# Kernel tuning notes

Hardware: AMD Instinct MI355X
Metric: run time of the kernel (lower is better)

The kernel has to match this reference:

```python
import jax, jax.numpy as jnp
import numpy as np

B, S, H, E = 8, 512, 1024, 8
T = B * S            # total tokens
CAP = T // E         # capacity, capacity_factor = 1.0


def _moe(x, wg, ew1, eb1, ew2, eb2):
    # x: [T, H] tokens; top-1 gating with capacity, DeepSpeed-style dispatch/combine
    gates = jax.nn.softmax(x @ wg)                      # [T, E]
    idx = jnp.argmax(gates, axis=-1)                    # [T]
    mask1 = jax.nn.one_hot(idx, E, dtype=x.dtype)       # [T, E]
    locations = jnp.cumsum(mask1, axis=0) - 1.0         # position within expert queue
    mask1 = mask1 * (locations < CAP).astype(x.dtype)   # drop overflow tokens
    gates1 = jnp.sum(gates * mask1, axis=-1)            # [T] combine weight
    locs = jnp.sum(locations * mask1, axis=-1).astype(jnp.int32)  # [T]
    loc_oh = jax.nn.one_hot(locs, CAP, dtype=x.dtype)   # [T, C]
    combine = gates1[:, None, None] * mask1[:, :, None] * loc_oh[:, None, :]  # [T,E,C]
    dispatch = (combine > 0).astype(x.dtype)            # [T, E, C]
    xd = jnp.einsum('sec,sm->ecm', dispatch, x)         # gather tokens per expert
    h = jnp.einsum('ecm,emn->ecn', xd, ew1) + eb1[:, None, :]
    h = jnp.einsum('ecn,enp->ecp', h, ew2) + eb2[:, None, :]
    return jnp.einsum('sec,ecm->sm', combine, h)        # scatter back, weighted


def setup_inputs() -> dict:
    key = jax.random.key(0)
    ks = jax.random.split(key, 16)
    w = lambda k, shape: jax.random.normal(k, shape, jnp.float32) * 0.02
    return {
        'x': jax.random.normal(ks[0], (B, S, H), jnp.float32),
        'y': jax.random.randint(ks[1], (B,), 0, H),
        'w1': w(ks[2], (H, H)), 'b1': jnp.zeros((H,), jnp.float32),
        'w2': w(ks[3], (H, H)), 'b2': jnp.zeros((H,), jnp.float32),
        'w3': w(ks[4], (H, H)), 'b3': jnp.zeros((H,), jnp.float32),
        'wg1': w(ks[5], (H, E)),
        'e1_w1': w(ks[6], (E, H, H)), 'e1_b1': jnp.zeros((E, H), jnp.float32),
        'e1_w2': w(ks[7], (E, H, H)), 'e1_b2': jnp.zeros((E, H), jnp.float32),
        'wg2': w(ks[8], (H, E)),
        'e2_w1': w(ks[9], (E, H, H)), 'e2_b1': jnp.zeros((E, H), jnp.float32),
        'e2_w2': w(ks[10], (E, H, H)), 'e2_b2': jnp.zeros((E, H), jnp.float32),
    }


def reference(x, y, w1, b1, w2, b2, w3, b3, wg1, e1_w1, e1_b1, e1_w2, e1_b2,
              wg2, e2_w1, e2_b1, e2_w2, e2_b2):
    xf = x.reshape(-1, H)                               # [T, H]
    hidden = xf @ w1 + b1
    out = _moe(hidden, wg1, e1_w1, e1_b1, e1_w2, e1_b2)
    out = out @ w2 + b2
    out = _moe(out, wg2, e2_w1, e2_b1, e2_w2, e2_b2)
    out = out @ w3 + b3
    hidden = hidden + out
    sent = hidden.reshape(B, S, H).mean(axis=1)         # [B, H] logits
    logp = jax.nn.log_softmax(sent, axis=-1)
    return -jnp.mean(logp[jnp.arange(B), y])
```

## Files before the change

### kernel.cpp

```cpp
#include <hip/hip_runtime.h>

#define TOK 4096
#define HID 1024
#define NEXP 8
#define CAP 512
#define WSZ 1048576

typedef _Float16 f16;
typedef f16 f16x8 __attribute__((ext_vector_type(8)));
typedef f16 f16x4 __attribute__((ext_vector_type(4)));
typedef f16 f16x2 __attribute__((ext_vector_type(2)));
typedef float f32x4 __attribute__((ext_vector_type(4)));

typedef const __attribute__((address_space(1))) void gvoid;
typedef __attribute__((address_space(3))) void lvoid;

__device__ __forceinline__ void gld16(const void* g, void* l) {
  __builtin_amdgcn_global_load_lds((gvoid*)g, (lvoid*)l, 16, 0, 0);
}

template<int MODE>
__global__ __launch_bounds__(512, 1) void gemm_fused(
    const f16* __restrict__ A, const f16* __restrict__ Bt,
    const float* __restrict__ bias, f16* __restrict__ C,
    const int* __restrict__ rowmap, const float* __restrict__ gmax,
    int rowsPerExpert, long bStride, int biasStride,
    const float* __restrict__ tsrc, f16* __restrict__ tdst, int nGemm)
{
  __shared__ __align__(16) unsigned char smem[65536];
  const int tid = threadIdx.x;

  if ((int)blockIdx.x >= nGemm) {
    float (*t)[65] = (float (*)[65])smem;
    const int tb = blockIdx.x - nGemm;
    const int mat = tb >> 7, t7 = tb & 127;
    const int nb = (t7 & 7) * 128, kb = (t7 >> 3) * 64;
    const float* src = tsrc + (size_t)mat * WSZ;
    f16* d = tdst + (size_t)mat * WSZ;
    const int half = tid >> 8, tl = tid & 255;
    const int rr = tl >> 4, c4 = (tl & 15) * 4;
    float (*th)[65] = t + half * 64;
    float4 v[4];
    #pragma unroll
    for (int p = 0; p < 4; ++p)
      v[p] = *(const float4*)&src[(size_t)(kb + p * 16 + rr) * HID + nb + half * 64 + c4];
    #pragma unroll
    for (int p = 0; p < 4; ++p) {
      th[p * 16 + rr][c4 + 0] = v[p].x;
      th[p * 16 + rr][c4 + 1] = v[p].y;
      th[p * 16 + rr][c4 + 2] = v[p].z;
      th[p * 16 + rr][c4 + 3] = v[p].w;
    }
    __syncthreads();
    #pragma unroll
    for (int it = 0; it < 2; ++it) {
      const int p = it * 256 + tl;
      const int n = p >> 3, kc = p & 7;
      f16x8 o;
      #pragma unroll
      for (int j = 0; j < 8; ++j) o[j] = (f16)th[kc * 8 + j][n];
      *(f16x8*)&d[(size_t)(nb + half * 64 + n) * HID + kb + kc * 8] = o;
    }
    return;
  }

  f16* As0 = (f16*)smem;
  f16* Bs0 = (f16*)(smem + 32768);
  const int w = tid >> 6, l = tid & 63;
  const int wr = w >> 2, wc = w & 3;

  const int orig = blockIdx.x;
  const int sw = (orig & 7) * 32 + (orig >> 3);
  const int bx = sw & 7, by = sw >> 3;
  const int e = (by * 128) / rowsPerExpert;

  const int lr = l >> 3;
  const int chunkSw = ((l & 7) ^ lr) * 8;

  const f16* pst[4];
  if (w < 4) {
    #pragma unroll
    for (int i = 0; i < 4; ++i) {
      int r = by * 128 + w * 32 + i * 8 + lr;
      long tok = r;
      if (MODE == 1) { int t = rowmap[r]; tok = (t < 0) ? (long)TOK : (long)t; }
      pst[i] = A + tok * HID + chunkSw;
    }
  } else {
    #pragma unroll
    for (int i = 0; i < 4; ++i)
      pst[i] = Bt + (size_t)e * bStride
             + (size_t)(bx * 128 + (w - 4) * 32 + i * 8 + lr) * HID + chunkSw;
  }

  f32x4 acc[4][2];
  #pragma unroll
  for (int i = 0; i < 4; ++i)
    #pragma unroll
    for (int j = 0; j < 2; ++j) acc[i][j] = (f32x4){0.f, 0.f, 0.f, 0.f};

  const int g = l >> 4, c = l & 15, sa = c & 7;

  {
    f16* db = (w < 4) ? As0 + (w * 32) * 64 : Bs0 + ((w - 4) * 32) * 64;
    #pragma unroll
    for (int i = 0; i < 4; ++i) gld16(pst[i], db + i * 8 * 64);
  }

  int cur = 0;
  for (int t = 0; t < 15; ++t) {
    {
      const int k0 = (t + 1) * 64;
      f16* db = (w < 4) ? As0 + ((cur ^ 1) * 8192) + (w * 32) * 64
                        : Bs0 + ((cur ^ 1) * 8192) + ((w - 4) * 32) * 64;
      #pragma unroll
      for (int i = 0; i < 4; ++i) gld16(pst[i] + k0, db + i * 8 * 64);
    }
    asm volatile("s_waitcnt vmcnt(4)" ::: "memory");
    asm volatile("s_barrier" ::: "memory");
    __builtin_amdgcn_s_setprio(1);
    #pragma unroll
    for (int h = 0; h < 2; ++h) {
      const int q = ((h * 4 + g) ^ sa) * 8;
      f16x8 af[4], bf[2];
      #pragma unroll
      for (int mi = 0; mi < 4; ++mi)
        af[mi] = *(const f16x8*)&As0[cur * 8192 + (wr * 64 + mi * 16 + c) * 64 + q];
      #pragma unroll
      for (int ni = 0; ni < 2; ++ni)
        bf[ni] = *(const f16x8*)&Bs0[cur * 8192 + (wc * 32 + ni * 16 + c) * 64 + q];
      #pragma unroll
      for (int mi = 0; mi < 4; ++mi)
        #pragma unroll
        for (int ni = 0; ni < 2; ++ni)
          acc[mi][ni] = __builtin_amdgcn_mfma_f32_16x16x32_f16(
              af[mi], bf[ni], acc[mi][ni], 0, 0, 0);
    }
    __builtin_amdgcn_s_setprio(0);
    asm volatile("s_barrier" ::: "memory");
    cur ^= 1;
  }
  asm volatile("s_waitcnt vmcnt(0)" ::: "memory");
  asm volatile("s_barrier" ::: "memory");
  __builtin_amdgcn_s_setprio(1);
  #pragma unroll
  for (int h = 0; h < 2; ++h) {
    const int q = ((h * 4 + g) ^ sa) * 8;
    f16x8 af[4], bf[2];
    #pragma unroll
    for (int mi = 0; mi < 4; ++mi)
      af[mi] = *(const f16x8*)&As0[cur * 8192 + (wr * 64 + mi * 16 + c) * 64 + q];
    #pragma unroll
    for (int ni = 0; ni < 2; ++ni)
      bf[ni] = *(const f16x8*)&Bs0[cur * 8192 + (wc * 32 + ni * 16 + c) * 64 + q];
    #pragma unroll
    for (int mi = 0; mi < 4; ++mi)
      #pragma unroll
      for (int ni = 0; ni < 2; ++ni)
        acc[mi][ni] = __builtin_amdgcn_mfma_f32_16x16x32_f16(
            af[mi], bf[ni], acc[mi][ni], 0, 0, 0);
  }
  __builtin_amdgcn_s_setprio(0);

  int tk[4][4];
  float gv[4][4];
  if (MODE == 2) {
    #pragma unroll
    for (int mi = 0; mi < 4; ++mi)
      #pragma unroll
      for (int rr = 0; rr < 4; ++rr) {
        int r = by * 128 + wr * 64 + mi * 16 + g * 4 + rr;
        int t = rowmap[r];
        tk[mi][rr] = t;
        gv[mi][rr] = (t >= 0) ? gmax[t] : 0.f;
      }
  }
  #pragma unroll
  for (int ni = 0; ni < 2; ++ni) {
    const int col = bx * 128 + wc * 32 + ni * 16 + c;
    const float bv = bias[(size_t)e * biasStride + col];
    #pragma unroll
    for (int mi = 0; mi < 4; ++mi) {
      #pragma unroll
      for (int rr = 0; rr < 4; ++rr) {
        const float v = acc[mi][ni][rr] + bv;
        if (MODE == 2) {
          if (tk[mi][rr] >= 0)
            C[(size_t)tk[mi][rr] * HID + col] = (f16)(v * gv[mi][rr]);
        } else {
          const int row = by * 128 + wr * 64 + mi * 16 + g * 4 + rr;
          C[(size_t)row * HID + col] = (f16)v;
        }
      }
    }
  }
}

__global__ __launch_bounds__(256, 8) void tcast3(
    const float* __restrict__ w1, const float* __restrict__ w2,
    const float* __restrict__ w3, f16* __restrict__ dst)
{
  __shared__ float t[64][65];
  const int z = blockIdx.z;
  const float* src = (z == 0) ? w1 : (z == 1) ? w2 : w3;
  f16* d = dst + (size_t)z * WSZ;
  const int tid = threadIdx.x;
  const int kb = blockIdx.y * 64, nb = blockIdx.x * 64;
  const int rr = tid >> 4, c4 = (tid & 15) * 4;
  float4 v[4];
  #pragma unroll
  for (int p = 0; p < 4; ++p)
    v[p] = *(const float4*)&src[(size_t)(kb + p * 16 + rr) * HID + nb + c4];
  #pragma unroll
  for (int p = 0; p < 4; ++p) {
    t[p * 16 + rr][c4 + 0] = v[p].x;
    t[p * 16 + rr][c4 + 1] = v[p].y;
    t[p * 16 + rr][c4 + 2] = v[p].z;
    t[p * 16 + rr][c4 + 3] = v[p].w;
  }
  __syncthreads();
  #pragma unroll
  for (int half = 0; half < 2; ++half) {
    const int p = half * 256 + tid;
    const int n = p >> 3, kc = p & 7;
    f16x8 o;
    #pragma unroll
    for (int j = 0; j < 8; ++j) o[j] = (f16)t[kc * 8 + j][n];
    *(f16x8*)&d[(size_t)(nb + n) * HID + kb + kc * 8] = o;
  }
}

__global__ void prep(const float* __restrict__ x, f16* __restrict__ X0,
                     f16* __restrict__ c1, f16* __restrict__ c2,
                     f16* __restrict__ p1, f16* __restrict__ p2) {
  const size_t i = (size_t)blockIdx.x * 256 + threadIdx.x;
  float4 v = *(const float4*)&x[i * 4];
  f16x4 o = {(f16)v.x, (f16)v.y, (f16)v.z, (f16)v.w};
  *(f16x4*)&X0[i * 4] = o;
  const f16x8 zz = {0, 0, 0, 0, 0, 0, 0, 0};
  if (i < 524288) { ((f16x8*)c1)[i] = zz; ((f16x8*)c2)[i] = zz; }
  if (i < 128)    { ((f16x8*)p1)[i] = zz; ((f16x8*)p2)[i] = zz; }
}

__global__ __launch_bounds__(256) void gate_kernel(
    const f16* __restrict__ act, const float* __restrict__ wg,
    int* __restrict__ idx, float* __restrict__ gmax)
{
  const int tid = threadIdx.x;
  const int tok = blockIdx.x * 8 + (tid >> 5);
  const int sl = tid & 31;
  const f16* row = act + (size_t)tok * HID + sl * 32;
  float xv[32];
  #pragma unroll
  for (int v = 0; v < 4; ++v) {
    f16x8 hv = *(const f16x8*)(row + v * 8);
    #pragma unroll
    for (int j = 0; j < 8; ++j) xv[v * 8 + j] = (float)hv[j];
  }
  float p[NEXP];
  #pragma unroll
  for (int e = 0; e < NEXP; ++e) p[e] = 0.f;
  const float* wr_ = wg + (size_t)(sl * 32) * NEXP;
  #pragma unroll
  for (int j = 0; j < 32; ++j) {
    #pragma unroll
    for (int e = 0; e < NEXP; ++e) p[e] += xv[j] * wr_[j * NEXP + e];
  }
  #pragma unroll
  for (int m = 1; m < 32; m <<= 1) {
    #pragma unroll
    for (int e = 0; e < NEXP; ++e) p[e] += __shfl_xor(p[e], m, 64);
  }
  if (sl == 0) {
    float mx = p[0]; int am = 0;
    #pragma unroll
    for (int e = 1; e < NEXP; ++e)
      if (p[e] > mx) { mx = p[e]; am = e; }
    float s = 0.f;
    #pragma unroll
    for (int e = 0; e < NEXP; ++e) s += expf(p[e] - mx);
    idx[tok] = am;
    gmax[tok] = 1.f / s;
  }
}

__global__ __launch_bounds__(512) void scan_kernel(
    const int* __restrict__ idx, int* __restrict__ rowmap)
{
  __shared__ int sidx[TOK];
  const int tid = threadIdx.x;
  for (int i = tid; i < TOK; i += 512) sidx[i] = idx[i];
  for (int i = tid; i < NEXP * CAP; i += 512) rowmap[i] = -1;
  __syncthreads();
  const int wave = tid >> 6, lane = tid & 63;
  int running = 0;
  for (int ch = 0; ch < TOK / 64; ++ch) {
    int t = ch * 64 + lane;
    bool flag = (sidx[t] == wave);
    unsigned long long m = __ballot(flag);
    int pos = running + __popcll(m & ((1ull << lane) - 1ull));
    if (flag && pos < CAP) rowmap[wave * CAP + pos] = t;
    running += __popcll(m);
  }
}

__global__ __launch_bounds__(256) void mean1_kernel(
    const f16* __restrict__ a, const f16* __restrict__ c,
    float* __restrict__ partial)
{
  const int h2 = blockIdx.x * 256 + threadIdx.x;
  const int b = blockIdx.y, sc = blockIdx.z;
  const f16x2* pa = (const f16x2*)(a + ((size_t)b * 512 + sc * 32) * HID) + h2;
  const f16x2* pc = (const f16x2*)(c + ((size_t)b * 512 + sc * 32) * HID) + h2;
  float a0 = 0.f, a1 = 0.f;
  #pragma unroll 4
  for (int s = 0; s < 32; ++s) {
    f16x2 va = pa[(size_t)s * 512];
    f16x2 vc = pc[(size_t)s * 512];
    a0 += (float)va[0] + (float)vc[0];
    a1 += (float)va[1] + (float)vc[1];
  }
  float* o = partial + ((size_t)sc * 8 + b) * HID;
  o[h2 * 2]     = a0;
  o[h2 * 2 + 1] = a1;
}

__global__ __launch_bounds__(256) void mean2_kernel(
    const float* __restrict__ partial, float* __restrict__ sent)
{
  const int h2 = blockIdx.x * 256 + threadIdx.x;
  const int b = blockIdx.y;
  float a0 = 0.f, a1 = 0.f;
  #pragma unroll
  for (int sc = 0; sc < 16; ++sc) {
    const float* p = partial + ((size_t)sc * 8 + b) * HID + h2 * 2;
    a0 += p[0]; a1 += p[1];
  }
  sent[b * HID + h2 * 2]     = a0 * (1.f / 512.f);
  sent[b * HID + h2 * 2 + 1] = a1 * (1.f / 512.f);
}

__global__ __launch_bounds__(1024) void loss_kernel(
    const float* __restrict__ sent, const int* __restrict__ y,
    float* __restrict__ out)
{
  __shared__ float red[1024];
  float loss = 0.0f;
  for (int b = 0; b < 8; ++b) {
    float v = sent[b * HID + threadIdx.x];
    red[threadIdx.x] = v;
    __syncthreads();
    for (int s = 512; s > 0; s >>= 1) {
      if (threadIdx.x < s)
        red[threadIdx.x] = fmaxf(red[threadIdx.x], red[threadIdx.x + s]);
      __syncthreads();
    }
    float m = red[0];
    __syncthreads();
    red[threadIdx.x] = expf(v - m);
    __syncthreads();
    for (int s = 512; s > 0; s >>= 1) {
      if (threadIdx.x < s) red[threadIdx.x] += red[threadIdx.x + s];
      __syncthreads();
    }
    if (threadIdx.x == 0) {
      float lse = m + logf(red[0]);
      loss += -(sent[b * HID + y[b]] - lse);
    }
    __syncthreads();
  }
  if (threadIdx.x == 0) out[0] = loss * (1.0f / 8.0f);
}

extern "C" void kernel_launch(void* const* d_in, const int* in_sizes, int n_in,
                              void* d_out, int out_size, void* d_ws, size_t ws_size,
                              hipStream_t stream)
{
  const float* x    = (const float*)d_in[0];
  const int*   y    = (const int*)d_in[1];
  const float* w1   = (const float*)d_in[2];
  const float* b1   = (const float*)d_in[3];
  const float* w2   = (const float*)d_in[4];
  const float* b2   = (const float*)d_in[5];
  const float* w3   = (const float*)d_in[6];
  const float* b3   = (const float*)d_in[7];
  const float* wg1  = (const float*)d_in[8];
  const float* e1w1 = (const float*)d_in[9];
  const float* e1b1 = (const float*)d_in[10];
  const float* e1w2 = (const float*)d_in[11];
  const float* e1b2 = (const float*)d_in[12];
  const float* wg2  = (const float*)d_in[13];
  const float* e2w1 = (const float*)d_in[14];
  const float* e2b1 = (const float*)d_in[15];
  const float* e2w2 = (const float*)d_in[16];
  const float* e2b2 = (const float*)d_in[17];

  f16* WT = (f16*)d_ws;
  f16* X0 = WT + (size_t)35 * WSZ;
  f16* H  = X0 + (size_t)TOK * HID;
  f16* EA = H + (size_t)(TOK + 1) * HID;
  f16* C1 = EA + (size_t)TOK * HID;
  f16* M1 = C1 + (size_t)TOK * HID;
  f16* C2 = M1 + (size_t)(TOK + 1) * HID;
  f16* O  = C2 + (size_t)TOK * HID;
  float* gmax  = (float*)(O + (size_t)TOK * HID);
  int* idx     = (int*)(gmax + TOK);
  int* rowmap  = idx + TOK;
  float* sent  = (float*)(rowmap + TOK);
  float* partial = sent + 8 * HID;

  f16* WTe1a = WT + (size_t)3 * WSZ;
  f16* WTe1b = WT + (size_t)11 * WSZ;
  f16* WTe2a = WT + (size_t)19 * WSZ;
  f16* WTe2b = WT + (size_t)27 * WSZ;

  const int FUSED = 256 + 8 * 128;

  prep<<<4096, 256, 0, stream>>>(x, X0, C1, C2,
                                 H + (size_t)TOK * HID, M1 + (size_t)TOK * HID);
  tcast3<<<dim3(16, 16, 3), 256, 0, stream>>>(w1, w2, w3, WT);

  gemm_fused<0><<<FUSED, 512, 0, stream>>>(X0, WT, b1, H, nullptr, nullptr,
                                           TOK, 0, 0, e1w1, WTe1a, 256);

  gate_kernel<<<512, 256, 0, stream>>>(H, wg1, idx, gmax);
  scan_kernel<<<1, 512, 0, stream>>>(idx, rowmap);
  gemm_fused<1><<<FUSED, 512, 0, stream>>>(H, WTe1a, e1b1, EA, rowmap, nullptr,
                                           CAP, WSZ, HID, e1w2, WTe1b, 256);
  gemm_fused<2><<<FUSED, 512, 0, stream>>>(EA, WTe1b, e1b2, C1, rowmap, gmax,
                                           CAP, WSZ, HID, e2w1, WTe2a, 256);

  gemm_fused<0><<<FUSED, 512, 0, stream>>>(C1, WT + (size_t)1 * WSZ, b2, M1,
                                           nullptr, nullptr, TOK, 0, 0,
                                           e2w2, WTe2b, 256);

  gate_kernel<<<512, 256, 0, stream>>>(M1, wg2, idx, gmax);
  scan_kernel<<<1, 512, 0, stream>>>(idx, rowmap);
  gemm_fused<1><<<256, 512, 0, stream>>>(M1, WTe2a, e2b1, EA, rowmap, nullptr,
                                         CAP, WSZ, HID, w1, WT, 256);
  gemm_fused<2><<<256, 512, 0, stream>>>(EA, WTe2b, e2b2, C2, rowmap, gmax,
                                         CAP, WSZ, HID, w1, WT, 256);

  gemm_fused<0><<<256, 512, 0, stream>>>(C2, WT + (size_t)2 * WSZ, b3, O,
                                         nullptr, nullptr, TOK, 0, 0,
                                         w1, WT, 256);

  mean1_kernel<<<dim3(2, 8, 16), 256, 0, stream>>>(H, O, partial);
  mean2_kernel<<<dim3(2, 8), 256, 0, stream>>>(partial, sent);
  loss_kernel<<<1, 1024, 0, stream>>>(sent, y, (float*)d_out);
}
```

Baseline: 223.4 us.

## Apply final linear layer after sequence mean and merge prep kernels

Because the mean over the sequence is linear, the final out@w3+b3 GEMM over all 4096 tokens is replaced by averaging C2 per batch first and multiplying the 8 mean vectors by w3 in a small sent_kernel. The prep and weight-transpose kernels are merged into one launch, the gate kernel loads gate weights as float4, and the loss kernel uses wave shuffles instead of a shared-memory tree. This removes a full 4096x1024x1024 GEMM plus the O buffer and two launches. Summation order changes slightly, and sent_kernel does a serial 1024-long dot product per thread with few blocks.

```diff
diff --git a/kernel.cpp b/kernel.cpp
--- a/kernel.cpp
+++ b/kernel.cpp
@@ -196,16 +196,33 @@
   }
 }
 
-__global__ __launch_bounds__(256, 8) void tcast3(
+__global__ __launch_bounds__(256) void prep2(
+    const float* __restrict__ x, f16* __restrict__ X0,
+    f16* __restrict__ c1, f16* __restrict__ c2,
+    f16* __restrict__ p1, f16* __restrict__ p2,
     const float* __restrict__ w1, const float* __restrict__ w2,
-    const float* __restrict__ w3, f16* __restrict__ dst)
+    const float* __restrict__ w3, f16* __restrict__ WT)
 {
   __shared__ float t[64][65];
-  const int z = blockIdx.z;
+  const int tid = threadIdx.x;
+  if ((int)blockIdx.x < 2048) {
+    const f16x8 zz = {0, 0, 0, 0, 0, 0, 0, 0};
+    #pragma unroll
+    for (int it = 0; it < 2; ++it) {
+      const size_t i = (size_t)blockIdx.x * 256 + tid + (size_t)it * 524288;
+      float4 v = *(const float4*)&x[i * 4];
+      f16x4 o = {(f16)v.x, (f16)v.y, (f16)v.z, (f16)v.w};
+      *(f16x4*)&X0[i * 4] = o;
+      if (i < 524288) { ((f16x8*)c1)[i] = zz; ((f16x8*)c2)[i] = zz; }
+      if (i < 128)    { ((f16x8*)p1)[i] = zz; ((f16x8*)p2)[i] = zz; }
+    }
+    return;
+  }
+  const int zb = blockIdx.x - 2048;
+  const int z = zb >> 8, t7 = zb & 255;
   const float* src = (z == 0) ? w1 : (z == 1) ? w2 : w3;
-  f16* d = dst + (size_t)z * WSZ;
-  const int tid = threadIdx.x;
-  const int kb = blockIdx.y * 64, nb = blockIdx.x * 64;
+  f16* d = WT + (size_t)z * WSZ;
+  const int kb = (t7 >> 4) * 64, nb = (t7 & 15) * 64;
   const int rr = tid >> 4, c4 = (tid & 15) * 4;
   float4 v[4];
   #pragma unroll
@@ -230,18 +247,6 @@
   }
 }
 
-__global__ void prep(const float* __restrict__ x, f16* __restrict__ X0,
-                     f16* __restrict__ c1, f16* __restrict__ c2,
-                     f16* __restrict__ p1, f16* __restrict__ p2) {
-  const size_t i = (size_t)blockIdx.x * 256 + threadIdx.x;
-  float4 v = *(const float4*)&x[i * 4];
-  f16x4 o = {(f16)v.x, (f16)v.y, (f16)v.z, (f16)v.w};
-  *(f16x4*)&X0[i * 4] = o;
-  const f16x8 zz = {0, 0, 0, 0, 0, 0, 0, 0};
-  if (i < 524288) { ((f16x8*)c1)[i] = zz; ((f16x8*)c2)[i] = zz; }
-  if (i < 128)    { ((f16x8*)p1)[i] = zz; ((f16x8*)p2)[i] = zz; }
-}
-
 __global__ __launch_bounds__(256) void gate_kernel(
     const f16* __restrict__ act, const float* __restrict__ wg,
     int* __restrict__ idx, float* __restrict__ gmax)
@@ -260,11 +265,14 @@
   float p[NEXP];
   #pragma unroll
   for (int e = 0; e < NEXP; ++e) p[e] = 0.f;
-  const float* wr_ = wg + (size_t)(sl * 32) * NEXP;
+  const float4* w4 = (const float4*)(wg + (size_t)(sl * 32) * NEXP);
   #pragma unroll
   for (int j = 0; j < 32; ++j) {
-    #pragma unroll
-    for (int e = 0; e < NEXP; ++e) p[e] += xv[j] * wr_[j * NEXP + e];
+    float4 lo = w4[2 * j], hi = w4[2 * j + 1];
+    p[0] += xv[j] * lo.x; p[1] += xv[j] * lo.y;
+    p[2] += xv[j] * lo.z; p[3] += xv[j] * lo.w;
+    p[4] += xv[j] * hi.x; p[5] += xv[j] * hi.y;
+    p[6] += xv[j] * hi.z; p[7] += xv[j] * hi.w;
   }
   #pragma unroll
   for (int m = 1; m < 32; m <<= 1) {
@@ -304,72 +312,97 @@
   }
 }
 
-__global__ __launch_bounds__(256) void mean1_kernel(
-    const f16* __restrict__ a, const f16* __restrict__ c,
-    float* __restrict__ partial)
+__global__ __launch_bounds__(256) void meanHC_kernel(
+    const f16* __restrict__ Hb, const f16* __restrict__ C2b,
+    float* __restrict__ pH, float* __restrict__ pC)
 {
   const int h2 = blockIdx.x * 256 + threadIdx.x;
   const int b = blockIdx.y, sc = blockIdx.z;
-  const f16x2* pa = (const f16x2*)(a + ((size_t)b * 512 + sc * 32) * HID) + h2;
-  const f16x2* pc = (const f16x2*)(c + ((size_t)b * 512 + sc * 32) * HID) + h2;
-  float a0 = 0.f, a1 = 0.f;
+  const f16x2* pa = (const f16x2*)(Hb + ((size_t)b * 512 + sc * 32) * HID) + h2;
+  const f16x2* pc = (const f16x2*)(C2b + ((size_t)b * 512 + sc * 32) * HID) + h2;
+  float a0 = 0.f, a1 = 0.f, c0 = 0.f, c1 = 0.f;
   #pragma unroll 4
   for (int s = 0; s < 32; ++s) {
     f16x2 va = pa[(size_t)s * 512];
     f16x2 vc = pc[(size_t)s * 512];
-    a0 += (float)va[0] + (float)vc[0];
-    a1 += (float)va[1] + (float)vc[1];
-  }
-  float* o = partial + ((size_t)sc * 8 + b) * HID;
-  o[h2 * 2]     = a0;
-  o[h2 * 2 + 1] = a1;
-}
-
-__global__ __launch_bounds__(256) void mean2_kernel(
-    const float* __restrict__ partial, float* __restrict__ sent)
-{
-  const int h2 = blockIdx.x * 256 + threadIdx.x;
-  const int b = blockIdx.y;
-  float a0 = 0.f, a1 = 0.f;
-  #pragma unroll
-  for (int sc = 0; sc < 16; ++sc) {
-    const float* p = partial + ((size_t)sc * 8 + b) * HID + h2 * 2;
-    a0 += p[0]; a1 += p[1];
-  }
-  sent[b * HID + h2 * 2]     = a0 * (1.f / 512.f);
-  sent[b * HID + h2 * 2 + 1] = a1 * (1.f / 512.f);
+    a0 += (float)va[0]; a1 += (float)va[1];
+    c0 += (float)vc[0]; c1 += (float)vc[1];
+  }
+  float* oh = pH + ((size_t)sc * 8 + b) * HID;
+  float* oc = pC + ((size_t)sc * 8 + b) * HID;
+  oh[h2 * 2] = a0; oh[h2 * 2 + 1] = a1;
+  oc[h2 * 2] = c0; oc[h2 * 2 + 1] = c1;
+}
+
+__global__ __launch_bounds__(256) void sent_kernel(
+    const float* __restrict__ pH, const float* __restrict__ pC,
+    const f16* __restrict__ WT2, const float* __restrict__ b3,
+    float* __restrict__ sent)
+{
+  __shared__ float c2m[HID];
+  const int tid = threadIdx.x;
+  const int b = blockIdx.x >> 2, ch = blockIdx.x & 3;
+  for (int kk = tid; kk < HID; kk += 256) {
+    float s = 0.f;
+    #pragma unroll
+    for (int sc = 0; sc < 16; ++sc) s += pC[((size_t)sc * 8 + b) * HID + kk];
+    c2m[kk] = s * (1.f / 512.f);
+  }
+  __syncthreads();
+  const int col = ch * 256 + tid;
+  float hv = 0.f;
+  #pragma unroll
+  for (int sc = 0; sc < 16; ++sc) hv += pH[((size_t)sc * 8 + b) * HID + col];
+  float acc = hv * (1.f / 512.f) + b3[col];
+  const f16* wrow = WT2 + (size_t)col * HID;
+  for (int k0 = 0; k0 < HID; k0 += 8) {
+    f16x8 wv = *(const f16x8*)(wrow + k0);
+    #pragma unroll
+    for (int j = 0; j < 8; ++j) acc += c2m[k0 + j] * (float)wv[j];
+  }
+  sent[b * HID + col] = acc;
 }
 
 __global__ __launch_bounds__(1024) void loss_kernel(
     const float* __restrict__ sent, const int* __restrict__ y,
     float* __restrict__ out)
 {
-  __shared__ float red[1024];
+  __shared__ float red[17];
+  const int tid = threadIdx.x;
+  const int wid = tid >> 6, lane = tid & 63;
   float loss = 0.0f;
   for (int b = 0; b < 8; ++b) {
-    float v = sent[b * HID + threadIdx.x];
-    red[threadIdx.x] = v;
-    __syncthreads();
-    for (int s = 512; s > 0; s >>= 1) {
-      if (threadIdx.x < s)
-        red[threadIdx.x] = fmaxf(red[threadIdx.x], red[threadIdx.x + s]);
-      __syncthreads();
-    }
-    float m = red[0];
-    __syncthreads();
-    red[threadIdx.x] = expf(v - m);
-    __syncthreads();
-    for (int s = 512; s > 0; s >>= 1) {
-      if (threadIdx.x < s) red[threadIdx.x] += red[threadIdx.x + s];
-      __syncthreads();
-    }
-    if (threadIdx.x == 0) {
-      float lse = m + logf(red[0]);
-      loss += -(sent[b * HID + y[b]] - lse);
-    }
-    __syncthreads();
-  }
-  if (threadIdx.x == 0) out[0] = loss * (1.0f / 8.0f);
+    const float v = sent[b * HID + tid];
+    float m = v;
+    #pragma unroll
+    for (int o = 32; o; o >>= 1) m = fmaxf(m, __shfl_xor(m, o, 64));
+    if (lane == 0) red[wid] = m;
+    __syncthreads();
+    if (tid < 16) {
+      float mm = red[tid];
+      #pragma unroll
+      for (int o = 8; o; o >>= 1) mm = fmaxf(mm, __shfl_xor(mm, o, 16));
+      if (tid == 0) red[16] = mm;
+    }
+    __syncthreads();
+    const float M = red[16];
+    float s = expf(v - M);
+    #pragma unroll
+    for (int o = 32; o; o >>= 1) s += __shfl_xor(s, o, 64);
+    __syncthreads();
+    if (lane == 0) red[wid] = s;
+    __syncthreads();
+    if (tid < 16) {
+      float ss = red[tid];
+      #pragma unroll
+      for (int o = 8; o; o >>= 1) ss += __shfl_xor(ss, o, 16);
+      if (tid == 0) red[16] = M + logf(ss);
+    }
+    __syncthreads();
+    if (tid == 0) loss += -(sent[b * HID + y[b]] - red[16]);
+    __syncthreads();
+  }
+  if (tid == 0) out[0] = loss * (1.0f / 8.0f);
 }
 
 extern "C" void kernel_launch(void* const* d_in, const int* in_sizes, int n_in,
@@ -402,12 +435,12 @@
   f16* C1 = EA + (size_t)TOK * HID;
   f16* M1 = C1 + (size_t)TOK * HID;
   f16* C2 = M1 + (size_t)(TOK + 1) * HID;
-  f16* O  = C2 + (size_t)TOK * HID;
-  float* gmax  = (float*)(O + (size_t)TOK * HID);
+  float* gmax  = (float*)(C2 + (size_t)TOK * HID);
   int* idx     = (int*)(gmax + TOK);
   int* rowmap  = idx + TOK;
   float* sent  = (float*)(rowmap + TOK);
-  float* partial = sent + 8 * HID;
+  float* pH    = sent + 8 * HID;
+  float* pC    = pH + 16 * 8 * HID;
 
   f16* WTe1a = WT + (size_t)3 * WSZ;
   f16* WTe1b = WT + (size_t)11 * WSZ;
@@ -416,9 +449,9 @@
 
   const int FUSED = 256 + 8 * 128;
 
-  prep<<<4096, 256, 0, stream>>>(x, X0, C1, C2,
-                                 H + (size_t)TOK * HID, M1 + (size_t)TOK * HID);
-  tcast3<<<dim3(16, 16, 3), 256, 0, stream>>>(w1, w2, w3, WT);
+  prep2<<<2816, 256, 0, stream>>>(x, X0, C1, C2,
+                                  H + (size_t)TOK * HID, M1 + (size_t)TOK * HID,
+                                  w1, w2, w3, WT);
 
   gemm_fused<0><<<FUSED, 512, 0, stream>>>(X0, WT, b1, H, nullptr, nullptr,
                                            TOK, 0, 0, e1w1, WTe1a, 256);
@@ -441,11 +474,7 @@
   gemm_fused<2><<<256, 512, 0, stream>>>(EA, WTe2b, e2b2, C2, rowmap, gmax,
                                          CAP, WSZ, HID, w1, WT, 256);
 
-  gemm_fused<0><<<256, 512, 0, stream>>>(C2, WT + (size_t)2 * WSZ, b3, O,
-                                         nullptr, nullptr, TOK, 0, 0,
-                                         w1, WT, 256);
-
-  mean1_kernel<<<dim3(2, 8, 16), 256, 0, stream>>>(H, O, partial);
-  mean2_kernel<<<dim3(2, 8), 256, 0, stream>>>(partial, sent);
+  meanHC_kernel<<<dim3(2, 8, 16), 256, 0, stream>>>(H, C2, pH, pC);
+  sent_kernel<<<32, 256, 0, stream>>>(pH, pC, WT + (size_t)2 * WSZ, b3, sent);
   loss_kernel<<<1, 1024, 0, stream>>>(sent, y, (float*)d_out);
 }
```

Result: faster. 218.4 us (-2.3%).
